# Kernel optimization log

Measured on AMD Instinct MI355X. Metric: run time of the kernel, lower is better.

## Reference

```python
import jax, jax.numpy as jnp
import numpy as np

N, K, C, J = 200000, 512, 64, 32  # nodes, node feature dim, mixture components (Ccurr+1), macrostates


def setup_inputs() -> dict:
    key = jax.random.key(0)
    k0, k1, k2, k3, k4, k5 = jax.random.split(key, 6)
    x = jax.random.normal(k0, (N, K), dtype=jnp.float32)
    macrostate = jax.random.randint(k1, (N,), 0, J)  # macrostate_assignments (int, constant)
    # Gaussian emission parameters theta[k] (diagonal covariance), one per component
    mu = jax.random.normal(k2, (C, K), dtype=jnp.float32)
    log_var = 0.1 * jax.random.normal(k3, (C, K), dtype=jnp.float32)
    # stick-breaking weights beta (positive, sums to 1) and CRF counts njk (non-negative)
    b = jax.random.uniform(k4, (C,), dtype=jnp.float32) + 1e-3
    beta = b / b.sum()
    njk = 100.0 * jax.random.uniform(k5, (J, C), dtype=jnp.float32)
    alpha = jnp.float32(1.0)
    return {"x": x, "mu": mu, "log_var": log_var, "beta": beta, "njk": njk,
            "alpha": alpha, "macrostate": macrostate}


def reference(x, mu, log_var, beta, njk, alpha, macrostate):
    # f_X_theta_log[u, k] = theta[k].get_data_log_likelihood(x[u])  (diagonal Gaussian)
    # expand ||(x - mu)/sigma||^2 as a GEMM to stay compute-bound:
    inv_var = jnp.exp(-log_var)                                   # [C, K]
    quad = ((x * x) @ inv_var.T                                   # [N, C]
            - 2.0 * (x @ (mu * inv_var).T)
            + jnp.sum(mu * mu * inv_var, axis=1))
    log_norm = jnp.sum(log_var, axis=1) + x.shape[1] * jnp.log(2.0 * jnp.pi)
    f_log = -0.5 * (quad + log_norm)                              # [N, C]
    # per-node: unnorm_log_p_zu = log(alpha*beta + njk[j]) + f_X_theta_log[u]
    prior_log = jnp.log(alpha * beta[None, :] + njk)              # [J, C]
    logits = prior_log[macrostate] + f_log                        # [N, C]
    # p_zu via numerically-stable softmax; posterior_matrix[u] += p_zu
    posterior = jax.nn.softmax(logits, axis=1)
    return posterior
```

## Files before the change

kernel.cpp:

```cpp
#include <hip/hip_runtime.h>
#include <hip/hip_bf16.h>

typedef _Float16 f16;
typedef _Float16 f16x8 __attribute__((ext_vector_type(8)));
typedef float f32x4 __attribute__((ext_vector_type(4)));

#define NN 200000
#define KK 512
#define CC 64
#define JJ 32
#define WFRAG_ELEMS (48 * 4 * 64 * 8)

__device__ inline void gload_lds16(const void* g, void* l) {
  __builtin_amdgcn_global_load_lds(
      (const __attribute__((address_space(1))) void*)g,
      (__attribute__((address_space(3))) void*)l, 16, 0, 0);
}

__global__ __launch_bounds__(256) void fill_w(const float* __restrict__ mu,
                                              const float* __restrict__ lv,
                                              f16* __restrict__ wfrag) {
  int idx = blockIdx.x * 256 + threadIdx.x;
  int i = idx & 7, l = (idx >> 3) & 63, ct = (idx >> 9) & 3, kF = idx >> 11;
  int k = (kF & 15) * 32 + (l >> 4) * 8 + i;
  int c = ct * 16 + (l & 15);
  int sec = kF >> 4;
  float lvv = lv[c * KK + k];
  float w;
  if (sec == 0) {
    w = -0.5f * expm1f(-lvv);
  } else {
    float w2 = mu[c * KK + k] * expf(-lvv);
    float wh = (float)(f16)w2;
    w = (sec == 1) ? wh : (w2 - wh);
  }
  wfrag[idx] = (f16)w;
}

__global__ __launch_bounds__(64) void fill_bias(const float* __restrict__ mu,
                                                const float* __restrict__ lv,
                                                const float* __restrict__ beta,
                                                const float* __restrict__ njk,
                                                const float* __restrict__ alphap,
                                                float* __restrict__ bias) {
  int c = blockIdx.x;
  int lane = threadIdx.x;
  float s = 0.0f;
  for (int k = lane; k < KK; k += 64) {
    float l2 = lv[c * KK + k];
    float m = mu[c * KK + k];
    s += fmaf(m * m, expf(-l2), l2);
  }
  #pragma unroll
  for (int d = 1; d < 64; d <<= 1) s += __shfl_xor(s, d, 64);
  float base = -0.5f * (s + 512.0f * 1.8378770664093453f);
  if (lane < JJ)
    bias[lane * CC + c] = logf(alphap[0] * beta[c] + njk[lane * CC + c]) + base;
}

__global__ __launch_bounds__(256, 3) void gmm_main(
    const float* __restrict__ x, const int* __restrict__ ms,
    const f16* __restrict__ wfrag, const float* __restrict__ bias,
    float* __restrict__ out) {
  __shared__ char lds[2 * 12288];
  const int t = threadIdx.x;
  const int lane = t & 63;
  const int wv = t >> 6;
  const int lr = lane & 15;
  const int kg = lane >> 4;
  const long row0 = (long)blockIdx.x * 128 + wv * 32;
  const bool valid = row0 < NN;
  const long r0 = valid ? row0 + lr : 0;
  const long r1 = valid ? row0 + 16 + lr : 0;

  const float* xp0 = x + r0 * KK + kg * 8;
  const float* xp1 = x + r1 * KK + kg * 8;
  const char* wfb = (const char*)wfrag;
  const int lsec = wv * 1024 + lane * 16;

  f32x4 acc[2][4];
  #pragma unroll
  for (int rt = 0; rt < 2; ++rt)
    #pragma unroll
    for (int ct = 0; ct < 4; ++ct) acc[rt][ct] = (f32x4)0.0f;

  #pragma unroll
  for (int sec = 0; sec < 3; ++sec)
    gload_lds16(wfb + sec * 65536 + lsec, lds + sec * 4096 + wv * 1024);

  f32x4 cx[4];
  cx[0] = __builtin_nontemporal_load(reinterpret_cast<const f32x4*>(xp0));
  cx[1] = __builtin_nontemporal_load(reinterpret_cast<const f32x4*>(xp0 + 4));
  cx[2] = __builtin_nontemporal_load(reinterpret_cast<const f32x4*>(xp1));
  cx[3] = __builtin_nontemporal_load(reinterpret_cast<const f32x4*>(xp1 + 4));
  __syncthreads();

  int cur = 0;
  #pragma unroll 1
  for (int s = 0; s < 16; ++s) {
    f32x4 nx[4];
    if (s < 15) {
      const char* gsrc = wfb + (s + 1) * 4096;
      char* ldst = lds + (cur ^ 1) * 12288;
      #pragma unroll
      for (int sec = 0; sec < 3; ++sec)
        gload_lds16(gsrc + sec * 65536 + lsec, ldst + sec * 4096 + wv * 1024);
      const float* p0 = xp0 + (s + 1) * 32;
      const float* p1 = xp1 + (s + 1) * 32;
      nx[0] = __builtin_nontemporal_load(reinterpret_cast<const f32x4*>(p0));
      nx[1] = __builtin_nontemporal_load(reinterpret_cast<const f32x4*>(p0 + 4));
      nx[2] = __builtin_nontemporal_load(reinterpret_cast<const f32x4*>(p1));
      nx[3] = __builtin_nontemporal_load(reinterpret_cast<const f32x4*>(p1 + 4));
    }

    f16x8 fxx[2], fxh[2], fxl[2];
    #pragma unroll
    for (int rt = 0; rt < 2; ++rt) {
      #pragma unroll
      for (int i = 0; i < 8; ++i) {
        float v = (i < 4) ? cx[rt * 2][i] : cx[rt * 2 + 1][i - 4];
        f16 h = (f16)v;
        fxh[rt][i] = h;
        fxl[rt][i] = (f16)(v - (float)h);
        fxx[rt][i] = (f16)(v * v);
      }
    }

    const f16* lbase = (const f16*)(lds + cur * 12288) + lane * 8;
    #pragma unroll
    for (int ct = 0; ct < 4; ++ct) {
      f16x8 bw1 = *reinterpret_cast<const f16x8*>(lbase + ct * 512);
      f16x8 bwh = *reinterpret_cast<const f16x8*>(lbase + 2048 + ct * 512);
      f16x8 bwl = *reinterpret_cast<const f16x8*>(lbase + 4096 + ct * 512);
      #pragma unroll
      for (int rt = 0; rt < 2; ++rt) {
        acc[rt][ct] = __builtin_amdgcn_mfma_f32_16x16x32_f16(fxx[rt], bw1, acc[rt][ct], 0, 0, 0);
        acc[rt][ct] = __builtin_amdgcn_mfma_f32_16x16x32_f16(fxh[rt], bwh, acc[rt][ct], 0, 0, 0);
        acc[rt][ct] = __builtin_amdgcn_mfma_f32_16x16x32_f16(fxh[rt], bwl, acc[rt][ct], 0, 0, 0);
        acc[rt][ct] = __builtin_amdgcn_mfma_f32_16x16x32_f16(fxl[rt], bwh, acc[rt][ct], 0, 0, 0);
      }
    }

    __syncthreads();
    cur ^= 1;
    if (s < 15) {
      cx[0] = nx[0]; cx[1] = nx[1]; cx[2] = nx[2]; cx[3] = nx[3];
    }
  }

  if (valid) {
    #pragma unroll
    for (int rt = 0; rt < 2; ++rt) {
      long rbase = row0 + rt * 16 + kg * 4;
      #pragma unroll
      for (int r = 0; r < 4; ++r) {
        int j = ms[rbase + r];
        const float* bj = bias + j * CC + lr;
        float v0 = acc[rt][0][r] + bj[0];
        float v1 = acc[rt][1][r] + bj[16];
        float v2 = acc[rt][2][r] + bj[32];
        float v3 = acc[rt][3][r] + bj[48];
        float m = fmaxf(fmaxf(v0, v1), fmaxf(v2, v3));
        #pragma unroll
        for (int d = 1; d < 16; d <<= 1) m = fmaxf(m, __shfl_xor(m, d, 64));
        float e0 = __expf(v0 - m), e1 = __expf(v1 - m);
        float e2 = __expf(v2 - m), e3 = __expf(v3 - m);
        float sum = (e0 + e1) + (e2 + e3);
        #pragma unroll
        for (int d = 1; d < 16; d <<= 1) sum += __shfl_xor(sum, d, 64);
        float inv = 1.0f / sum;
        float* o = out + (size_t)rbase * CC + r * CC + lr;
        __builtin_nontemporal_store(e0 * inv, o);
        __builtin_nontemporal_store(e1 * inv, o + 16);
        __builtin_nontemporal_store(e2 * inv, o + 32);
        __builtin_nontemporal_store(e3 * inv, o + 48);
      }
    }
  }
}

extern "C" void kernel_launch(void* const* d_in, const int* in_sizes, int n_in,
                              void* d_out, int out_size, void* d_ws, size_t ws_size,
                              hipStream_t stream) {
  const float* x     = (const float*)d_in[0];
  const float* mu    = (const float*)d_in[1];
  const float* lv    = (const float*)d_in[2];
  const float* beta  = (const float*)d_in[3];
  const float* njk   = (const float*)d_in[4];
  const float* alpha = (const float*)d_in[5];
  const int*   ms    = (const int*)d_in[6];
  float* out = (float*)d_out;

  f16* wfrag  = (f16*)d_ws;
  float* bias = (float*)((char*)d_ws + WFRAG_ELEMS * sizeof(f16));

  fill_w<<<WFRAG_ELEMS / 256, 256, 0, stream>>>(mu, lv, wfrag);
  fill_bias<<<CC, 64, 0, stream>>>(mu, lv, beta, njk, alpha, bias);
  gmm_main<<<(NN + 127) / 128, 256, 0, stream>>>(x, ms, wfrag, bias, out);
}
```

Before: 129.8 us.

## Deepen x prefetch to two stages with manual vmcnt waits and barriers

Restructures the main K loop into a two-step unrolled body with two register buffers for x, so x loads are issued two stages ahead instead of one. The __syncthreads is replaced by an explicit s_waitcnt vmcnt(4) plus s_barrier with sched barriers, so only the older loads are waited on while the next x loads stay in flight. The intent is to hide global-load latency for x behind the MFMA work. In exchange the last stages issue redundant clamped loads, register pressure rises, and the hand-counted vmcnt values must match the compiler's actual load ordering to stay correct.

```diff
diff --git a/kernel.cpp b/kernel.cpp
--- a/kernel.cpp
+++ b/kernel.cpp
@@ -15,6 +15,10 @@
   __builtin_amdgcn_global_load_lds(
       (const __attribute__((address_space(1))) void*)g,
       (__attribute__((address_space(3))) void*)l, 16, 0, 0);
+}
+
+__device__ inline f32x4 ntl(const float* p) {
+  return __builtin_nontemporal_load(reinterpret_cast<const f32x4*>(p));
 }
 
 __global__ __launch_bounds__(256) void fill_w(const float* __restrict__ mu,
@@ -84,49 +88,49 @@
     #pragma unroll
     for (int ct = 0; ct < 4; ++ct) acc[rt][ct] = (f32x4)0.0f;
 
+  f32x4 xA[4], xB[4];
+
   #pragma unroll
   for (int sec = 0; sec < 3; ++sec)
     gload_lds16(wfb + sec * 65536 + lsec, lds + sec * 4096 + wv * 1024);
-
-  f32x4 cx[4];
-  cx[0] = __builtin_nontemporal_load(reinterpret_cast<const f32x4*>(xp0));
-  cx[1] = __builtin_nontemporal_load(reinterpret_cast<const f32x4*>(xp0 + 4));
-  cx[2] = __builtin_nontemporal_load(reinterpret_cast<const f32x4*>(xp1));
-  cx[3] = __builtin_nontemporal_load(reinterpret_cast<const f32x4*>(xp1 + 4));
-  __syncthreads();
-
-  int cur = 0;
-  #pragma unroll 1
-  for (int s = 0; s < 16; ++s) {
-    f32x4 nx[4];
-    if (s < 15) {
-      const char* gsrc = wfb + (s + 1) * 4096;
-      char* ldst = lds + (cur ^ 1) * 12288;
+  xA[0] = ntl(xp0);      xA[1] = ntl(xp0 + 4);
+  xA[2] = ntl(xp1);      xA[3] = ntl(xp1 + 4);
+  xB[0] = ntl(xp0 + 32); xB[1] = ntl(xp0 + 36);
+  xB[2] = ntl(xp1 + 32); xB[3] = ntl(xp1 + 36);
+  asm volatile("s_waitcnt vmcnt(8)" ::: "memory");
+  __builtin_amdgcn_sched_barrier(0);
+  __builtin_amdgcn_s_barrier();
+  __builtin_amdgcn_sched_barrier(0);
+
+  auto step = [&](int s, int PAR, f32x4 (&xs)[4]) {
+    {
+      const int sn = (s + 1 < 16) ? s + 1 : 15;
+      const char* gsrc = wfb + sn * 4096;
+      char* ldst = lds + (PAR ^ 1) * 12288;
       #pragma unroll
       for (int sec = 0; sec < 3; ++sec)
         gload_lds16(gsrc + sec * 65536 + lsec, ldst + sec * 4096 + wv * 1024);
-      const float* p0 = xp0 + (s + 1) * 32;
-      const float* p1 = xp1 + (s + 1) * 32;
-      nx[0] = __builtin_nontemporal_load(reinterpret_cast<const f32x4*>(p0));
-      nx[1] = __builtin_nontemporal_load(reinterpret_cast<const f32x4*>(p0 + 4));
-      nx[2] = __builtin_nontemporal_load(reinterpret_cast<const f32x4*>(p1));
-      nx[3] = __builtin_nontemporal_load(reinterpret_cast<const f32x4*>(p1 + 4));
-    }
-
+    }
     f16x8 fxx[2], fxh[2], fxl[2];
     #pragma unroll
     for (int rt = 0; rt < 2; ++rt) {
       #pragma unroll
       for (int i = 0; i < 8; ++i) {
-        float v = (i < 4) ? cx[rt * 2][i] : cx[rt * 2 + 1][i - 4];
+        float v = (i < 4) ? xs[rt * 2][i] : xs[rt * 2 + 1][i - 4];
         f16 h = (f16)v;
         fxh[rt][i] = h;
         fxl[rt][i] = (f16)(v - (float)h);
         fxx[rt][i] = (f16)(v * v);
       }
     }
-
-    const f16* lbase = (const f16*)(lds + cur * 12288) + lane * 8;
+    {
+      const int sx = (s + 2 < 16) ? s + 2 : 15;
+      const float* p0 = xp0 + sx * 32;
+      const float* p1 = xp1 + sx * 32;
+      xs[0] = ntl(p0); xs[1] = ntl(p0 + 4);
+      xs[2] = ntl(p1); xs[3] = ntl(p1 + 4);
+    }
+    const f16* lbase = (const f16*)(lds + PAR * 12288) + lane * 8;
     #pragma unroll
     for (int ct = 0; ct < 4; ++ct) {
       f16x8 bw1 = *reinterpret_cast<const f16x8*>(lbase + ct * 512);
@@ -140,12 +144,16 @@
         acc[rt][ct] = __builtin_amdgcn_mfma_f32_16x16x32_f16(fxl[rt], bwh, acc[rt][ct], 0, 0, 0);
       }
     }
-
-    __syncthreads();
-    cur ^= 1;
-    if (s < 15) {
-      cx[0] = nx[0]; cx[1] = nx[1]; cx[2] = nx[2]; cx[3] = nx[3];
-    }
+    asm volatile("s_waitcnt vmcnt(4)" ::: "memory");
+    __builtin_amdgcn_sched_barrier(0);
+    __builtin_amdgcn_s_barrier();
+    __builtin_amdgcn_sched_barrier(0);
+  };
+
+  #pragma unroll 1
+  for (int ss = 0; ss < 16; ss += 2) {
+    step(ss, 0, xA);
+    step(ss + 1, 1, xB);
   }
 
   if (valid) {
```

Result: slower. 138.3 us (+6.5%).
